# Optimization experiments

Measured on AMD Instinct MI355X. Metric: run time of the kernel, lower is better.

## Reference

```python
import jax, jax.numpy as jnp
import numpy as np

N = 50000      # nodes
E = 800000     # edges (pos and neg each)
IN = 128       # in_channels
HID = 64       # hidden_dim
H = 4          # heads
OUT = 64       # out_channels


def setup_inputs() -> dict:
    key = jax.random.key(0)
    ks = jax.random.split(key, 11)
    s = 0.05
    return {
        "x": jax.random.normal(ks[0], (N, IN), dtype=jnp.float32),
        "pos_edge_index": jax.random.randint(ks[1], (2, E), 0, N, dtype=jnp.int32),
        "neg_edge_index": jax.random.randint(ks[2], (2, E), 0, N, dtype=jnp.int32),
        # conv1 params: Linear [IN, H*HID], attention vectors [H, HID], bias [H*HID]
        "W1": jax.random.normal(ks[3], (IN, H * HID), dtype=jnp.float32) * s,
        "att_src1": jax.random.normal(ks[4], (H, HID), dtype=jnp.float32) * s,
        "att_dst1": jax.random.normal(ks[5], (H, HID), dtype=jnp.float32) * s,
        "b1": jax.random.normal(ks[6], (H * HID,), dtype=jnp.float32) * s,
        # conv2 params: heads=1
        "W2": jax.random.normal(ks[7], (H * HID, OUT), dtype=jnp.float32) * s,
        "att_src2": jax.random.normal(ks[8], (1, OUT), dtype=jnp.float32) * s,
        "att_dst2": jax.random.normal(ks[9], (1, OUT), dtype=jnp.float32) * s,
        "b2": jax.random.normal(ks[10], (OUT,), dtype=jnp.float32) * s,
    }


def gat_conv(x, edge_index, W, att_src, att_dst, bias, heads, ch):
    """PyG GATConv: add self-loops, per-head linear, leaky-relu edge score,
    scatter-softmax over target neighborhoods, scatter-add aggregation."""
    n = x.shape[0]
    loop = jnp.arange(n, dtype=edge_index.dtype)
    src = jnp.concatenate([edge_index[0], loop])  # message source j
    dst = jnp.concatenate([edge_index[1], loop])  # aggregation target i

    h = (x @ W).reshape(n, heads, ch)                      # [N, H, C]
    a_s = jnp.einsum("nhc,hc->nh", h, att_src)             # alpha from source
    a_d = jnp.einsum("nhc,hc->nh", h, att_dst)             # alpha from target

    alpha = jax.nn.leaky_relu(a_s[src] + a_d[dst], 0.2)    # [Etot, H]
    m = jax.ops.segment_max(alpha, dst, num_segments=n)    # per-target max
    e = jnp.exp(alpha - m[dst])
    denom = jax.ops.segment_sum(e, dst, num_segments=n)
    w = e / (denom[dst] + 1e-16)                           # softmax weights

    out = jax.ops.segment_sum(w[:, :, None] * h[src], dst, num_segments=n)
    return out.reshape(n, heads * ch) + bias


def reference(x, pos_edge_index, neg_edge_index,
              W1, att_src1, att_dst1, b1,
              W2, att_src2, att_dst2, b2):
    # encode
    z = jax.nn.relu(gat_conv(x, pos_edge_index, W1, att_src1, att_dst1, b1, H, HID))
    z = gat_conv(z, pos_edge_index, W2, att_src2, att_dst2, b2, 1, OUT)
    # decode: edge dot-product logits over pos + neg edges
    ei = jnp.concatenate([pos_edge_index, neg_edge_index], axis=-1)  # [2, 2E]
    logits = (z[ei[0]] * z[ei[1]]).sum(axis=-1)                      # [2E]
    return logits
```

## Files before the change

kernel.cpp:

```cpp
#include <hip/hip_runtime.h>
#include <hip/hip_bf16.h>
#include <math.h>

#define IN_CH 128
#define HID 64
#define HEADS 4
#define C1 (HEADS*HID)
#define OUT_CH 64

typedef __attribute__((ext_vector_type(8))) short short8v;
typedef __attribute__((ext_vector_type(4))) float f32x4;

__device__ __forceinline__ float lrelu(float x){ return x > 0.f ? x : 0.2f*x; }

__device__ __forceinline__ ushort f2b(float f){
  unsigned u = __builtin_bit_cast(unsigned, f);
  unsigned r = (u + 0x7FFF + ((u>>16)&1)) >> 16;
  return (ushort)r;
}
__device__ __forceinline__ float b2f(ushort b){
  unsigned u = ((unsigned)b) << 16;
  return __builtin_bit_cast(float, u);
}

__device__ __forceinline__ float wsum64(float v){
  #pragma unroll
  for (int m = 32; m >= 1; m >>= 1) v += __shfl_xor(v, m, 64);
  return v;
}

__device__ __forceinline__ float dot2(unsigned ua, unsigned ub){
  float la = __builtin_bit_cast(float, ua << 16);
  float ha = __builtin_bit_cast(float, ua & 0xFFFF0000u);
  float lb = __builtin_bit_cast(float, ub << 16);
  float hb = __builtin_bit_cast(float, ub & 0xFFFF0000u);
  return la*lb + ha*hb;
}

__device__ __forceinline__ void unpack8(uint4 u, float* v){
  v[0]=__builtin_bit_cast(float,u.x<<16); v[1]=__builtin_bit_cast(float,u.x&0xFFFF0000u);
  v[2]=__builtin_bit_cast(float,u.y<<16); v[3]=__builtin_bit_cast(float,u.y&0xFFFF0000u);
  v[4]=__builtin_bit_cast(float,u.z<<16); v[5]=__builtin_bit_cast(float,u.z&0xFFFF0000u);
  v[6]=__builtin_bit_cast(float,u.w<<16); v[7]=__builtin_bit_cast(float,u.w&0xFFFF0000u);
}


__global__ void k_blocksum(const int* __restrict__ deg, int* bsum, int n){
  __shared__ int buf[256];
  int b = blockIdx.x, tid = threadIdx.x;
  int i = b*256 + tid;
  buf[tid] = (i < n) ? deg[i] : 0;
  __syncthreads();
  for (int off = 128; off > 0; off >>= 1){
    if (tid < off) buf[tid] += buf[tid + off];
    __syncthreads();
  }
  if (tid == 0) bsum[b] = buf[0];
}

__global__ void k_scanb(int* bsum, int nb){
  __shared__ int buf[256];
  int tid = threadIdx.x;
  int v = (tid < nb) ? bsum[tid] : 0;
  buf[tid] = v;
  __syncthreads();
  for (int off = 1; off < 256; off <<= 1){
    int t = (tid >= off) ? buf[tid - off] : 0;
    __syncthreads();
    buf[tid] += t;
    __syncthreads();
  }
  if (tid < nb) bsum[tid] = buf[tid] - v;
}

__global__ void k_scanfinal(const int* __restrict__ deg, const int* __restrict__ bsum,
                            int* rowptr, int* cursor, ushort* csrc, int n){
  __shared__ int buf[256];
  int b = blockIdx.x, tid = threadIdx.x;
  int i = b*256 + tid;
  int v = (i < n) ? deg[i] : 0;
  buf[tid] = v;
  __syncthreads();
  for (int off = 1; off < 256; off <<= 1){
    int t = (tid >= off) ? buf[tid - off] : 0;
    __syncthreads();
    buf[tid] += t;
    __syncthreads();
  }
  if (i < n){
    int r = bsum[b] + buf[tid];
    rowptr[i + 1] = r;
    cursor[i] = r - v;
    csrc[r - 1] = (ushort)i;
  }
  if (b == 0 && tid == 0) rowptr[0] = 0;
}

__global__ void k_scatter(const int* __restrict__ src, const int* __restrict__ dst,
                          int* cursor, ushort* csrc, int e){
  int i = blockIdx.x*256 + threadIdx.x;
  if (i < e){
    int d = dst[i];
    int slot = atomicAdd(&cursor[d], 1);
    __builtin_nontemporal_store((ushort)src[i], csrc + slot);
  }
}

__global__ void k_setup(int* deg, const float* __restrict__ W1, ushort* __restrict__ W1t,
                        const float* __restrict__ W2, ushort* __restrict__ W2t,
                        const float* __restrict__ as1v, const float* __restrict__ ad1v,
                        const float* __restrict__ as2v, const float* __restrict__ ad2v,
                        float* was4, float* wad4, float* w2s, float* w2d, int n, int nb){
  int b = blockIdx.x, tid = threadIdx.x;
  if (b < nb){
    int i = b*256 + tid;
    if (i < n) deg[i] = 1;
  } else if (b < nb + 128){
    int i = (b - nb)*256 + tid;
    int k = i >> 8, c = i & 255;
    W1t[(size_t)c*IN_CH + k] = f2b(W1[i]);
  } else if (b < nb + 192){
    int i = (b - nb - 128)*256 + tid;
    int k = i >> 6, c = i & 63;
    W2t[(size_t)c*C1 + k] = f2b(W2[i]);
  } else if (b == nb + 192){
    #pragma unroll
    for (int r = 0; r < 2; ++r){
      int t = tid + r*256;
      int c = t >> 2, h = t & 3;
      float s = 0.f, d = 0.f;
      for (int j = 0; j < HID; ++j){
        float w = W1[c*C1 + h*HID + j];
        s += w * as1v[h*HID + j];
        d += w * ad1v[h*HID + j];
      }
      was4[t] = s; wad4[t] = d;
    }
  } else {
    float s = 0.f, d = 0.f;
    for (int o = 0; o < OUT_CH; ++o){
      float w = W2[tid*OUT_CH + o];
      s += w * as2v[o];
      d += w * ad2v[o];
    }
    w2s[tid] = s; w2d[tid] = d;
  }
}

__global__ __launch_bounds__(256) void k_histfatt(
    const int* __restrict__ dst, int* deg, int e, int eb,
    const float* __restrict__ x, const float* __restrict__ was4,
    const float* __restrict__ wad4, ushort* __restrict__ xb,
    float* __restrict__ as1, float* __restrict__ ad1, int n){
  int b = blockIdx.x;
  if (b < eb){
    int i = b*256 + threadIdx.x;
    if (i < e) atomicAdd(&deg[dst[i]], 1);
    return;
  }
  int i = (b - eb)*4 + (threadIdx.x >> 6);
  int l = threadIdx.x & 63;
  if (i >= n) return;
  float2 u = *(const float2*)(x + (size_t)i*IN_CH + 2*l);
  ushort2 o; o.x = f2b(u.x); o.y = f2b(u.y);
  *(ushort2*)(xb + (size_t)i*IN_CH + 2*l) = o;
  float v0 = u.x, v1 = u.y;
  f32x4 s0 = *(const f32x4*)(was4 + 8*l);
  f32x4 s1 = *(const f32x4*)(was4 + 8*l + 4);
  f32x4 d0 = *(const f32x4*)(wad4 + 8*l);
  f32x4 d1 = *(const f32x4*)(wad4 + 8*l + 4);
  f32x4 ps, pd;
  #pragma unroll
  for (int h = 0; h < 4; ++h){
    ps[h] = wsum64(v0*s0[h] + v1*s1[h]);
    pd[h] = wsum64(v0*d0[h] + v1*d1[h]);
  }
  if (l == 0){
    *(f32x4*)(as1 + 4*i) = ps;
    *(f32x4*)(ad1 + 4*i) = pd;
  }
}

__global__ __launch_bounds__(256) void k_fatt2(const ushort* __restrict__ z1b,
    const float* __restrict__ w2s, const float* __restrict__ w2d,
    float* __restrict__ as2, float* __restrict__ ad2, int n){
  int i = blockIdx.x*4 + (threadIdx.x >> 6);
  int l = threadIdx.x & 63;
  if (i >= n) return;
  ushort4 u = *(const ushort4*)(z1b + (size_t)i*C1 + 4*l);
  float v0 = b2f(u.x), v1 = b2f(u.y), v2 = b2f(u.z), v3 = b2f(u.w);
  f32x4 s = *(const f32x4*)(w2s + 4*l);
  f32x4 d = *(const f32x4*)(w2d + 4*l);
  float ps = wsum64(v0*s[0] + v1*s[1] + v2*s[2] + v3*s[3]);
  float pd = wsum64(v0*d[0] + v1*d[1] + v2*d[2] + v3*d[3]);
  if (l == 0){ as2[i] = ps; ad2[i] = pd; }
}

__global__ __launch_bounds__(256) void k_fagg1(
    const ushort* __restrict__ xb, const float* __restrict__ as1,
    const float* __restrict__ ad1, const int* __restrict__ rowptr,
    const ushort* __restrict__ csrc, ushort* __restrict__ xagg, int n)
{
  __shared__ float  s_w[16][4][17];
  __shared__ ushort s_src[16][16];
  int tid = threadIdx.x;
  int grp = tid >> 4, ln = tid & 15;
  int i = blockIdx.x*16 + grp;
  if (i >= n) return;
  int beg = rowptr[i], end = rowptr[i+1];
  f32x4 ad4 = *(const f32x4*)(ad1 + 4*i);

  f32x4 S = (f32x4)(0.f);
  f32x4 ev0 = (f32x4)(0.f), ev1 = (f32x4)(0.f);
  int sj0 = 0, sj1 = 0, it = 0;
  for (int sl = beg + ln; sl < end; sl += 16, ++it){
    int sj = csrc[sl];
    f32x4 a4 = *(const f32x4*)(as1 + 4*sj);
    f32x4 ev;
    #pragma unroll
    for (int h = 0; h < 4; ++h)
      ev[h] = __expf(fminf(lrelu(a4[h] + ad4[h]), 60.f));
    if (it == 0){ ev0 = ev; sj0 = sj; }
    else if (it == 1){ ev1 = ev; sj1 = sj; }
    #pragma unroll
    for (int h = 0; h < 4; ++h) S[h] += ev[h];
  }
  f32x4 rd;
  #pragma unroll
  for (int h = 0; h < 4; ++h){
    float sh = S[h];
    #pragma unroll
    for (int k = 8; k >= 1; k >>= 1) sh += __shfl_xor(sh, k, 16);
    rd[h] = 1.f/(sh + 1e-16f);
  }

  float acc[4][8] = {};
  int nch = (end - beg + 15) >> 4;
  for (int c = 0; c < nch; ++c){
    int cs = beg + c*16;
    int cn = min(16, end - cs);
    if (ln < cn){
      int sj; f32x4 ev;
      if (c == 0){ sj = sj0; ev = ev0; }
      else if (c == 1){ sj = sj1; ev = ev1; }
      else {
        sj = csrc[cs + ln];
        f32x4 a4 = *(const f32x4*)(as1 + 4*sj);
        #pragma unroll
        for (int h = 0; h < 4; ++h)
          ev[h] = __expf(fminf(lrelu(a4[h] + ad4[h]), 60.f));
      }
      s_src[grp][ln] = (ushort)sj;
      #pragma unroll
      for (int h = 0; h < 4; ++h)
        s_w[grp][h][ln] = ev[h] * rd[h];
    }
    int e = 0;
    if (cn >= 4){
      uint4 u0 = *(const uint4*)(xb + (size_t)s_src[grp][0]*IN_CH + ln*8);
      uint4 u1 = *(const uint4*)(xb + (size_t)s_src[grp][1]*IN_CH + ln*8);
      uint4 u2 = *(const uint4*)(xb + (size_t)s_src[grp][2]*IN_CH + ln*8);
      uint4 u3 = *(const uint4*)(xb + (size_t)s_src[grp][3]*IN_CH + ln*8);
      for (; e + 7 < cn; e += 4){
        uint4 n0 = *(const uint4*)(xb + (size_t)s_src[grp][e+4]*IN_CH + ln*8);
        uint4 n1 = *(const uint4*)(xb + (size_t)s_src[grp][e+5]*IN_CH + ln*8);
        uint4 n2 = *(const uint4*)(xb + (size_t)s_src[grp][e+6]*IN_CH + ln*8);
        uint4 n3 = *(const uint4*)(xb + (size_t)s_src[grp][e+7]*IN_CH + ln*8);
        float v0[8], v1[8], v2[8], v3[8];
        unpack8(u0, v0); unpack8(u1, v1); unpack8(u2, v2); unpack8(u3, v3);
        #pragma unroll
        for (int h = 0; h < 4; ++h){
          float w0 = s_w[grp][h][e],   w1 = s_w[grp][h][e+1];
          float w2 = s_w[grp][h][e+2], w3 = s_w[grp][h][e+3];
          #pragma unroll
          for (int cc = 0; cc < 8; ++cc)
            acc[h][cc] += w0*v0[cc] + w1*v1[cc] + w2*v2[cc] + w3*v3[cc];
        }
        u0 = n0; u1 = n1; u2 = n2; u3 = n3;
      }
      {
        float v0[8], v1[8], v2[8], v3[8];
        unpack8(u0, v0); unpack8(u1, v1); unpack8(u2, v2); unpack8(u3, v3);
        #pragma unroll
        for (int h = 0; h < 4; ++h){
          float w0 = s_w[grp][h][e],   w1 = s_w[grp][h][e+1];
          float w2 = s_w[grp][h][e+2], w3 = s_w[grp][h][e+3];
          #pragma unroll
          for (int cc = 0; cc < 8; ++cc)
            acc[h][cc] += w0*v0[cc] + w1*v1[cc] + w2*v2[cc] + w3*v3[cc];
        }
        e += 4;
      }
    }
    for (; e < cn; ++e){
      uint4 u = *(const uint4*)(xb + (size_t)s_src[grp][e]*IN_CH + ln*8);
      float v[8];
      unpack8(u, v);
      #pragma unroll
      for (int h = 0; h < 4; ++h){
        float w = s_w[grp][h][e];
        #pragma unroll
        for (int cc = 0; cc < 8; ++cc) acc[h][cc] += w*v[cc];
      }
    }
  }
  #pragma unroll
  for (int h = 0; h < 4; ++h){
    uint4 o;
    o.x = (unsigned)f2b(acc[h][0]) | ((unsigned)f2b(acc[h][1])<<16);
    o.y = (unsigned)f2b(acc[h][2]) | ((unsigned)f2b(acc[h][3])<<16);
    o.z = (unsigned)f2b(acc[h][4]) | ((unsigned)f2b(acc[h][5])<<16);
    o.w = (unsigned)f2b(acc[h][6]) | ((unsigned)f2b(acc[h][7])<<16);
    *(uint4*)(xagg + (size_t)i*512 + h*128 + ln*8) = o;
  }
}

__global__ __launch_bounds__(256) void k_fagg2(
    const ushort* __restrict__ h2b, const float* __restrict__ as2,
    const float* __restrict__ ad2, const int* __restrict__ rowptr,
    const ushort* __restrict__ csrc, const float* __restrict__ bias,
    ushort* __restrict__ z2b, int n)
{
  __shared__ float  s_w[16][17];
  __shared__ ushort s_src[16][16];
  int tid = threadIdx.x;
  int grp = tid >> 4, ln = tid & 15;
  int i = blockIdx.x*16 + grp;
  if (i >= n) return;
  int beg = rowptr[i], end = rowptr[i+1];
  float adv = ad2[i];

  float S = 0.f;
  float ev0 = 0.f, ev1 = 0.f;
  int sj0 = 0, sj1 = 0, it = 0;
  for (int sl = beg + ln; sl < end; sl += 16, ++it){
    int sj = csrc[sl];
    float ev = __expf(fminf(lrelu(as2[sj] + adv), 60.f));
    if (it == 0){ ev0 = ev; sj0 = sj; }
    else if (it == 1){ ev1 = ev; sj1 = sj; }
    S += ev;
  }
  #pragma unroll
  for (int k = 8; k >= 1; k >>= 1) S += __shfl_xor(S, k, 16);
  float rd = 1.f/(S + 1e-16f);

  float acc[4] = {};
  int nch = (end - beg + 15) >> 4;
  for (int c = 0; c < nch; ++c){
    int cs = beg + c*16;
    int cn = min(16, end - cs);
    if (ln < cn){
      int sj; float ev;
      if (c == 0){ sj = sj0; ev = ev0; }
      else if (c == 1){ sj = sj1; ev = ev1; }
      else { sj = csrc[cs + ln]; ev = __expf(fminf(lrelu(as2[sj] + adv), 60.f)); }
      s_src[grp][ln] = (ushort)sj;
      s_w[grp][ln] = ev * rd;
    }
    int e = 0;
    for (; e + 1 < cn; e += 2){
      int sjA = s_src[grp][e], sjB = s_src[grp][e+1];
      float wA = s_w[grp][e], wB = s_w[grp][e+1];
      ushort4 uA = *(const ushort4*)(h2b + (size_t)sjA*OUT_CH + ln*4);
      ushort4 uB = *(const ushort4*)(h2b + (size_t)sjB*OUT_CH + ln*4);
      acc[0] += wA*b2f(uA.x) + wB*b2f(uB.x);
      acc[1] += wA*b2f(uA.y) + wB*b2f(uB.y);
      acc[2] += wA*b2f(uA.z) + wB*b2f(uB.z);
      acc[3] += wA*b2f(uA.w) + wB*b2f(uB.w);
    }
    if (e < cn){
      int sj = s_src[grp][e];
      float w = s_w[grp][e];
      ushort4 u = *(const ushort4*)(h2b + (size_t)sj*OUT_CH + ln*4);
      acc[0] += w*b2f(u.x); acc[1] += w*b2f(u.y);
      acc[2] += w*b2f(u.z); acc[3] += w*b2f(u.w);
    }
  }
  ushort4 o;
  o.x = f2b(acc[0] + bias[ln*4]);
  o.y = f2b(acc[1] + bias[ln*4+1]);
  o.z = f2b(acc[2] + bias[ln*4+2]);
  o.w = f2b(acc[3] + bias[ln*4+3]);
  *(ushort4*)(z2b + (size_t)i*OUT_CH + ln*4) = o;
}

template<bool RELU_BIAS>
__global__ __launch_bounds__(256) void k_gemm2(
    const ushort* __restrict__ A, const ushort* __restrict__ Bt,
    ushort* __restrict__ Cb, const float* __restrict__ bias,
    int M, int K, int lda, int ldc, int aZ, int bZ, int cZ)
{
  constexpr int BM = 128, BN = 64, NF = 2;
  __shared__ uint4 As[BM*8];
  __shared__ uint4 Bs[BN*8];
  int tid = threadIdx.x;
  int wave = tid >> 6, lane = tid & 63;
  int wr = wave >> 1, wc = wave & 1;
  int bm = blockIdx.y * BM;
  int z = blockIdx.z;
  const ushort* Az = A + (size_t)z*aZ;
  const ushort* Bz = Bt + (size_t)z*bZ;
  int g = lane >> 4, lr = lane & 15;

  f32x4 acc[4][NF];
  #pragma unroll
  for (int m = 0; m < 4; ++m)
    #pragma unroll
    for (int n = 0; n < NF; ++n) acc[m][n] = (f32x4)(0.f);

  for (int k0 = 0; k0 < K; k0 += 64){
    for (int idx = tid; idx < BM*8; idx += 256){
      int r = idx >> 3, c = idx & 7;
      int gr = bm + r;
      uint4 v = make_uint4(0u,0u,0u,0u);
      if (gr < M) v = *(const uint4*)(Az + (size_t)gr*lda + k0 + c*8);
      As[r*8 + (c ^ (r & 7))] = v;
    }
    for (int idx = tid; idx < BN*8; idx += 256){
      int r = idx >> 3, c = idx & 7;
      uint4 v = *(const uint4*)(Bz + (size_t)r*K + k0 + c*8);
      Bs[r*8 + (c ^ (r & 7))] = v;
    }
    __syncthreads();
    #pragma unroll
    for (int kk = 0; kk < 2; ++kk){
      short8v af[4], bf[NF];
      #pragma unroll
      for (int m = 0; m < 4; ++m){
        int r = wr*64 + m*16 + lr;
        int c = kk*4 + g;
        af[m] = *(const short8v*)&As[r*8 + (c ^ (r & 7))];
      }
      #pragma unroll
      for (int n = 0; n < NF; ++n){
        int r = wc*32 + n*16 + lr;
        int c = kk*4 + g;
        bf[n] = *(const short8v*)&Bs[r*8 + (c ^ (r & 7))];
      }
      #pragma unroll
      for (int m = 0; m < 4; ++m)
        #pragma unroll
        for (int n = 0; n < NF; ++n)
          acc[m][n] = __builtin_amdgcn_mfma_f32_16x16x32_bf16(af[m], bf[n], acc[m][n], 0, 0, 0);
    }
    __syncthreads();
  }
  #pragma unroll
  for (int m = 0; m < 4; ++m){
    #pragma unroll
    for (int q = 0; q < 4; ++q){
      int row = bm + wr*64 + m*16 + g*4 + q;
      if (row < M){
        #pragma unroll
        for (int n = 0; n < NF; ++n){
          int col = wc*32 + n*16 + lr;
          float v = acc[m][n][q];
          if (RELU_BIAS) v = fmaxf(v + bias[cZ*z + col], 0.f);
          Cb[(size_t)row*ldc + cZ*z + col] = f2b(v);
        }
      }
    }
  }
}

__global__ void k_decode(const ushort* __restrict__ z2b, const int* __restrict__ pos,
                         const int* __restrict__ neg, float* __restrict__ out, int e){
  int g = blockIdx.x*256 + threadIdx.x;
  int hf = e >> 1;
  int k = g >> 3;
  int sub = g & 7;
  if (k >= hf) return;
  int a0 = __builtin_nontemporal_load(pos + k);
  int b0 = __builtin_nontemporal_load(pos + e + k);
  int a1 = __builtin_nontemporal_load(pos + k + hf);
  int b1 = __builtin_nontemporal_load(pos + e + k + hf);
  int a2 = __builtin_nontemporal_load(neg + k);
  int b2 = __builtin_nontemporal_load(neg + e + k);
  int a3 = __builtin_nontemporal_load(neg + k + hf);
  int b3 = __builtin_nontemporal_load(neg + e + k + hf);
  uint4 ua0 = *(const uint4*)(z2b + (size_t)a0*OUT_CH + sub*8);
  uint4 ub0 = *(const uint4*)(z2b + (size_t)b0*OUT_CH + sub*8);
  uint4 ua1 = *(const uint4*)(z2b + (size_t)a1*OUT_CH + sub*8);
  uint4 ub1 = *(const uint4*)(z2b + (size_t)b1*OUT_CH + sub*8);
  uint4 ua2 = *(const uint4*)(z2b + (size_t)a2*OUT_CH + sub*8);
  uint4 ub2 = *(const uint4*)(z2b + (size_t)b2*OUT_CH + sub*8);
  uint4 ua3 = *(const uint4*)(z2b + (size_t)a3*OUT_CH + sub*8);
  uint4 ub3 = *(const uint4*)(z2b + (size_t)b3*OUT_CH + sub*8);
  float p0 = dot2(ua0.x, ub0.x) + dot2(ua0.y, ub0.y) + dot2(ua0.z, ub0.z) + dot2(ua0.w, ub0.w);
  float p1 = dot2(ua1.x, ub1.x) + dot2(ua1.y, ub1.y) + dot2(ua1.z, ub1.z) + dot2(ua1.w, ub1.w);
  float p2 = dot2(ua2.x, ub2.x) + dot2(ua2.y, ub2.y) + dot2(ua2.z, ub2.z) + dot2(ua2.w, ub2.w);
  float p3 = dot2(ua3.x, ub3.x) + dot2(ua3.y, ub3.y) + dot2(ua3.z, ub3.z) + dot2(ua3.w, ub3.w);
  #pragma unroll
  for (int mm = 4; mm >= 1; mm >>= 1){
    p0 += __shfl_xor(p0, mm, 64);
    p1 += __shfl_xor(p1, mm, 64);
    p2 += __shfl_xor(p2, mm, 64);
    p3 += __shfl_xor(p3, mm, 64);
  }
  if (sub == 0){
    __builtin_nontemporal_store(p0, out + k);
    __builtin_nontemporal_store(p1, out + k + hf);
    __builtin_nontemporal_store(p2, out + e + k);
    __builtin_nontemporal_store(p3, out + e + k + hf);
  }
}

extern "C" void kernel_launch(void* const* d_in, const int* in_sizes, int n_in,
                              void* d_out, int out_size, void* d_ws, size_t ws_size,
                              hipStream_t stream) {
  const float* x        = (const float*)d_in[0];
  const int*   pos      = (const int*)d_in[1];
  const int*   neg      = (const int*)d_in[2];
  const float* W1       = (const float*)d_in[3];
  const float* att_src1 = (const float*)d_in[4];
  const float* att_dst1 = (const float*)d_in[5];
  const float* b1       = (const float*)d_in[6];
  const float* W2       = (const float*)d_in[7];
  const float* att_src2 = (const float*)d_in[8];
  const float* att_dst2 = (const float*)d_in[9];
  const float* b2       = (const float*)d_in[10];
  float* out = (float*)d_out;

  const int N = in_sizes[0] / IN_CH;
  const int E = in_sizes[1] / 2;
  const int NNZ = E + N;

  char* w = (char*)d_ws;
  ushort* xb   = (ushort*)w;  w += (size_t)N*IN_CH*2;
  ushort* xagg = (ushort*)w;  w += (size_t)N*512*2;
  ushort* z1b  = (ushort*)w;  w += (size_t)N*C1*2;
  float* as1   = (float*)w;   w += (size_t)N*4*4;
  float* ad1   = (float*)w;   w += (size_t)N*4*4;
  float* as2   = (float*)w;   w += (size_t)N*4;
  float* ad2   = (float*)w;   w += (size_t)N*4;
  ushort* W1t  = (ushort*)w;  w += (size_t)C1*IN_CH*2;
  ushort* W2t  = (ushort*)w;  w += (size_t)OUT_CH*C1*2;
  float* was4  = (float*)w;   w += 512*4;
  float* wad4  = (float*)w;   w += 512*4;
  float* w2s   = (float*)w;   w += 256*4;
  float* w2d   = (float*)w;   w += 256*4;
  int* deg     = (int*)w;     w += (size_t)N*4;
  int* rowptr  = (int*)w;     w += (size_t)(N+1)*4;
  int* cursor  = (int*)w;     w += (size_t)N*4;
  int* bsum    = (int*)w;     w += (size_t)256*4;
  ushort* csrc = (ushort*)w;  w += (size_t)NNZ*2;

  ushort* h2b = xagg;
  ushort* z2b = xagg + (size_t)N*OUT_CH;

  int eb = (E + 255)/256;
  int nb = (N + 255)/256;
  int fb = (N + 3)/4;
  const int* pdst = pos + E;

  k_setup<<<nb + 194, 256, 0, stream>>>(deg, W1, W1t, W2, W2t,
      att_src1, att_dst1, att_src2, att_dst2, was4, wad4, w2s, w2d, N, nb);
  k_histfatt<<<eb + fb, 256, 0, stream>>>(pdst, deg, E, eb,
      x, was4, wad4, xb, as1, ad1, N);
  k_blocksum<<<nb, 256, 0, stream>>>(deg, bsum, N);
  k_scanb<<<1, 256, 0, stream>>>(bsum, nb);
  k_scanfinal<<<nb, 256, 0, stream>>>(deg, bsum, rowptr, cursor, csrc, N);
  k_scatter<<<eb, 256, 0, stream>>>(pos, pdst, cursor, csrc, E);

  k_fagg1<<<(N + 15)/16, 256, 0, stream>>>(xb, as1, ad1, rowptr, csrc, xagg, N);

  {
    dim3 g(1, (N + 127)/128, 4);
    k_gemm2<true><<<g, 256, 0, stream>>>(xagg, W1t, z1b, b1,
        N, IN_CH, 512, C1, IN_CH, OUT_CH*IN_CH, OUT_CH);
  }
  k_fatt2<<<(N + 3)/4, 256, 0, stream>>>(z1b, w2s, w2d, as2, ad2, N);

  {
    dim3 g(1, (N + 127)/128, 1);
    k_gemm2<false><<<g, 256, 0, stream>>>(z1b, W2t, h2b, nullptr,
        N, C1, C1, OUT_CH, 0, 0, 0);
  }
  k_fagg2<<<(N + 15)/16, 256, 0, stream>>>(h2b, as2, ad2, rowptr, csrc, b2, z2b, N);

  int db = (int)(((size_t)(E/2)*8 + 255)/256);
  k_decode<<<db, 256, 0, stream>>>(z2b, pos, neg, out, E);
}
```

Before: 279.2 us.

## Build CSR with LDS-privatized slice histograms and deterministic shared-memory scatter

Replaces global-atomic degree histogram and global-atomic cursor scatter with per-block LDS histograms over node halves and edge slices, a per-node prefix across slices, and an LDS-cursor scatter. The goal is to remove contended global atomics during CSR construction. In exchange, every block reads its whole edge slice twice (once per half), the partial-count buffer grows, and only 128 blocks are launched, which may underuse the GPU. It also splits the fused histogram/feature-attention kernel into separate launches.

Result: faster. 266.5 us (-4.5%).

```diff
diff --git a/kernel.cpp b/kernel.cpp
--- a/kernel.cpp
+++ b/kernel.cpp
@@ -7,6 +7,8 @@
 #define HEADS 4
 #define C1 (HEADS*HID)
 #define OUT_CH 64
+#define NSL 64
+#define MAXNH 25024
 
 typedef __attribute__((ext_vector_type(8))) short short8v;
 typedef __attribute__((ext_vector_type(4))) float f32x4;
@@ -44,6 +46,46 @@
   v[6]=__builtin_bit_cast(float,u.w<<16); v[7]=__builtin_bit_cast(float,u.w&0xFFFF0000u);
 }
 
+
+__global__ __launch_bounds__(1024) void k_hist2(
+    const int* __restrict__ dst, unsigned* __restrict__ part, int e, int nh, int n){
+  __shared__ unsigned hist[MAXNH];
+  int b = blockIdx.x;
+  int half = b >> 6, slice = b & (NSL-1);
+  int base = half*nh;
+  int cnt = half ? (n - nh) : nh;
+  int tid = threadIdx.x;
+  for (int i = tid; i < cnt; i += 1024) hist[i] = 0u;
+  __syncthreads();
+  int ES = (e + NSL - 1) / NSL;
+  int es = slice*ES, ee = min(e, es + ES);
+  for (int t = es + tid; t < ee; t += 1024){
+    int d = dst[t];
+    if (d >= base && d < base + cnt) atomicAdd(&hist[d - base], 1u);
+  }
+  __syncthreads();
+  unsigned* pb = part + (size_t)b*nh;
+  for (int i = tid; i < cnt; i += 1024) pb[i] = hist[i];
+}
+
+__global__ void k_degred(unsigned* __restrict__ part, int* __restrict__ deg,
+                         int n, int nh){
+  int g = blockIdx.x*256 + threadIdx.x;
+  if (g >= n) return;
+  int half = (g >= nh) ? 1 : 0;
+  int i = g - half*nh;
+  unsigned v[NSL];
+  #pragma unroll
+  for (int s = 0; s < NSL; ++s)
+    v[s] = part[(size_t)(half*NSL + s)*nh + i];
+  unsigned run = 0;
+  #pragma unroll
+  for (int s = 0; s < NSL; ++s){
+    part[(size_t)(half*NSL + s)*nh + i] = run;
+    run += v[s];
+  }
+  deg[g] = (int)run + 1;
+}
 
 __global__ void k_blocksum(const int* __restrict__ deg, int* bsum, int n){
   __shared__ int buf[256];
@@ -74,7 +116,7 @@
 }
 
 __global__ void k_scanfinal(const int* __restrict__ deg, const int* __restrict__ bsum,
-                            int* rowptr, int* cursor, ushort* csrc, int n){
+                            int* rowptr, ushort* csrc, int n){
   __shared__ int buf[256];
   int b = blockIdx.x, tid = threadIdx.x;
   int i = b*256 + tid;
@@ -90,40 +132,51 @@
   if (i < n){
     int r = bsum[b] + buf[tid];
     rowptr[i + 1] = r;
-    cursor[i] = r - v;
     csrc[r - 1] = (ushort)i;
   }
   if (b == 0 && tid == 0) rowptr[0] = 0;
 }
 
-__global__ void k_scatter(const int* __restrict__ src, const int* __restrict__ dst,
-                          int* cursor, ushort* csrc, int e){
-  int i = blockIdx.x*256 + threadIdx.x;
-  if (i < e){
-    int d = dst[i];
-    int slot = atomicAdd(&cursor[d], 1);
-    __builtin_nontemporal_store((ushort)src[i], csrc + slot);
-  }
-}
-
-__global__ void k_setup(int* deg, const float* __restrict__ W1, ushort* __restrict__ W1t,
+__global__ __launch_bounds__(1024) void k_scatter2(
+    const int* __restrict__ src, const int* __restrict__ dst,
+    const int* __restrict__ rowptr, const unsigned* __restrict__ part,
+    ushort* __restrict__ csrc, int e, int nh, int n){
+  __shared__ unsigned cur[MAXNH];
+  int b = blockIdx.x;
+  int half = b >> 6, slice = b & (NSL-1);
+  int base = half*nh;
+  int cnt = half ? (n - nh) : nh;
+  int tid = threadIdx.x;
+  const unsigned* pb = part + (size_t)b*nh;
+  for (int i = tid; i < cnt; i += 1024)
+    cur[i] = (unsigned)rowptr[base + i] + pb[i];
+  __syncthreads();
+  int ES = (e + NSL - 1) / NSL;
+  int es = slice*ES, ee = min(e, es + ES);
+  for (int t = es + tid; t < ee; t += 1024){
+    int d = dst[t];
+    if (d >= base && d < base + cnt){
+      unsigned slot = atomicAdd(&cur[d - base], 1u);
+      __builtin_nontemporal_store((ushort)src[t], csrc + slot);
+    }
+  }
+}
+
+__global__ void k_setup(const float* __restrict__ W1, ushort* __restrict__ W1t,
                         const float* __restrict__ W2, ushort* __restrict__ W2t,
                         const float* __restrict__ as1v, const float* __restrict__ ad1v,
                         const float* __restrict__ as2v, const float* __restrict__ ad2v,
-                        float* was4, float* wad4, float* w2s, float* w2d, int n, int nb){
+                        float* was4, float* wad4, float* w2s, float* w2d){
   int b = blockIdx.x, tid = threadIdx.x;
-  if (b < nb){
+  if (b < 128){
     int i = b*256 + tid;
-    if (i < n) deg[i] = 1;
-  } else if (b < nb + 128){
-    int i = (b - nb)*256 + tid;
     int k = i >> 8, c = i & 255;
     W1t[(size_t)c*IN_CH + k] = f2b(W1[i]);
-  } else if (b < nb + 192){
-    int i = (b - nb - 128)*256 + tid;
+  } else if (b < 192){
+    int i = (b - 128)*256 + tid;
     int k = i >> 6, c = i & 63;
     W2t[(size_t)c*C1 + k] = f2b(W2[i]);
-  } else if (b == nb + 192){
+  } else if (b == 192){
     #pragma unroll
     for (int r = 0; r < 2; ++r){
       int t = tid + r*256;
@@ -147,18 +200,10 @@
   }
 }
 
-__global__ __launch_bounds__(256) void k_histfatt(
-    const int* __restrict__ dst, int* deg, int e, int eb,
-    const float* __restrict__ x, const float* __restrict__ was4,
-    const float* __restrict__ wad4, ushort* __restrict__ xb,
-    float* __restrict__ as1, float* __restrict__ ad1, int n){
-  int b = blockIdx.x;
-  if (b < eb){
-    int i = b*256 + threadIdx.x;
-    if (i < e) atomicAdd(&deg[dst[i]], 1);
-    return;
-  }
-  int i = (b - eb)*4 + (threadIdx.x >> 6);
+__global__ __launch_bounds__(256) void k_fattc(const float* __restrict__ x,
+    const float* __restrict__ was4, const float* __restrict__ wad4,
+    ushort* __restrict__ xb, float* __restrict__ as1, float* __restrict__ ad1, int n){
+  int i = blockIdx.x*4 + (threadIdx.x >> 6);
   int l = threadIdx.x & 63;
   if (i >= n) return;
   float2 u = *(const float2*)(x + (size_t)i*IN_CH + 2*l);
@@ -524,6 +569,7 @@
   const int N = in_sizes[0] / IN_CH;
   const int E = in_sizes[1] / 2;
   const int NNZ = E + N;
+  const int NH = (N + 1) / 2;
 
   char* w = (char*)d_ws;
   ushort* xb   = (ushort*)w;  w += (size_t)N*IN_CH*2;
@@ -541,26 +587,25 @@
   float* w2d   = (float*)w;   w += 256*4;
   int* deg     = (int*)w;     w += (size_t)N*4;
   int* rowptr  = (int*)w;     w += (size_t)(N+1)*4;
-  int* cursor  = (int*)w;     w += (size_t)N*4;
   int* bsum    = (int*)w;     w += (size_t)256*4;
+  unsigned* part = (unsigned*)w; w += (size_t)2*NSL*NH*4;
   ushort* csrc = (ushort*)w;  w += (size_t)NNZ*2;
 
   ushort* h2b = xagg;
   ushort* z2b = xagg + (size_t)N*OUT_CH;
 
-  int eb = (E + 255)/256;
   int nb = (N + 255)/256;
-  int fb = (N + 3)/4;
   const int* pdst = pos + E;
 
-  k_setup<<<nb + 194, 256, 0, stream>>>(deg, W1, W1t, W2, W2t,
-      att_src1, att_dst1, att_src2, att_dst2, was4, wad4, w2s, w2d, N, nb);
-  k_histfatt<<<eb + fb, 256, 0, stream>>>(pdst, deg, E, eb,
-      x, was4, wad4, xb, as1, ad1, N);
+  k_setup<<<194, 256, 0, stream>>>(W1, W1t, W2, W2t,
+      att_src1, att_dst1, att_src2, att_dst2, was4, wad4, w2s, w2d);
+  k_hist2<<<2*NSL, 1024, 0, stream>>>(pdst, part, E, NH, N);
+  k_degred<<<nb, 256, 0, stream>>>(part, deg, N, NH);
+  k_fattc<<<(N + 3)/4, 256, 0, stream>>>(x, was4, wad4, xb, as1, ad1, N);
   k_blocksum<<<nb, 256, 0, stream>>>(deg, bsum, N);
   k_scanb<<<1, 256, 0, stream>>>(bsum, nb);
-  k_scanfinal<<<nb, 256, 0, stream>>>(deg, bsum, rowptr, cursor, csrc, N);
-  k_scatter<<<eb, 256, 0, stream>>>(pos, pdst, cursor, csrc, E);
+  k_scanfinal<<<nb, 256, 0, stream>>>(deg, bsum, rowptr, csrc, N);
+  k_scatter2<<<2*NSL, 1024, 0, stream>>>(pos, pdst, rowptr, part, csrc, E, NH, N);
 
   k_fagg1<<<(N + 15)/16, 256, 0, stream>>>(xb, as1, ad1, rowptr, csrc, xagg, N);
 
```
